# Performance work log

Hardware: AMD Instinct MI355X
Metric: run time of the kernel (lower is better)

## Reference

```python
import jax, jax.numpy as jnp
import numpy as np
import math

D_MODEL, D_K, N_HEADS = 1024, 64, 16
N, T = 2, 2048


def setup_inputs() -> dict:
    key = jax.random.key(0)
    ks = jax.random.split(key, 12)
    s = 1.0 / math.sqrt(D_MODEL)
    dh = D_K * N_HEADS
    return {
        "k": jax.random.normal(ks[0], (N, T, D_MODEL), jnp.float32),
        "q": jax.random.normal(ks[1], (N, T, D_MODEL), jnp.float32),
        "v": jax.random.normal(ks[2], (N, T, D_MODEL), jnp.float32),
        "mask": jnp.ones((N, T), jnp.int32),
        "Wk": jax.random.normal(ks[3], (D_MODEL, dh), jnp.float32) * s,
        "bk": jnp.zeros((dh,), jnp.float32),
        "Wq": jax.random.normal(ks[4], (D_MODEL, dh), jnp.float32) * s,
        "bq": jnp.zeros((dh,), jnp.float32),
        "Wv": jax.random.normal(ks[5], (D_MODEL, dh), jnp.float32) * s,
        "bv": jnp.zeros((dh,), jnp.float32),
        "Wo": jax.random.normal(ks[6], (dh, D_MODEL), jnp.float32) * (1.0 / math.sqrt(dh)),
        "bo": jnp.zeros((D_MODEL,), jnp.float32),
    }


def reference(k, q, v, mask, Wk, bk, Wq, bq, Wv, bv, Wo, bo):
    n, t = k.shape[0], k.shape[1]
    # project and split heads -> (N, H, T, d_k)
    K = (k @ Wk + bk).reshape(n, t, N_HEADS, D_K).transpose(0, 2, 1, 3)
    Q = (q @ Wq + bq).reshape(n, t, N_HEADS, D_K).transpose(0, 2, 1, 3)
    V = (v @ Wv + bv).reshape(n, t, N_HEADS, D_K).transpose(0, 2, 1, 3)
    scores = jnp.einsum("bhqd,bhkd->bhqk", Q, K) / math.sqrt(D_K)
    scores = jnp.where(mask[:, None, None, :] == 0, -jnp.inf, scores)
    weights = jax.nn.softmax(scores, axis=-1)
    A = jnp.einsum("bhqk,bhkd->bhqd", weights, V)
    A = A.transpose(0, 2, 1, 3).reshape(n, t, N_HEADS * D_K)
    return A @ Wo + bo
```

## Files before the change

### kernel.cpp

```cpp
#include <hip/hip_runtime.h>


typedef __bf16 bf16;
typedef __bf16 bf16x8 __attribute__((ext_vector_type(8)));
typedef __bf16 bf16x4 __attribute__((ext_vector_type(4)));
typedef float f32x4 __attribute__((ext_vector_type(4)));

#define MFMA16(a, b, c) __builtin_amdgcn_mfma_f32_16x16x32_bf16((a), (b), (c), 0, 0, 0)

__device__ __forceinline__ void load_lds16(const bf16* g, bf16* l) {
  __builtin_amdgcn_global_load_lds(
      (const __attribute__((address_space(1))) unsigned int*)g,
      (__attribute__((address_space(3))) unsigned int*)l, 16, 0, 0);
}

__device__ __forceinline__ bf16x8 cvt8(const float* __restrict__ p) {
  const f32x4 a = *(const f32x4*)p;
  const f32x4 b = *(const f32x4*)(p + 4);
  bf16x8 r;
  r[0] = (bf16)a[0]; r[1] = (bf16)a[1]; r[2] = (bf16)a[2]; r[3] = (bf16)a[3];
  r[4] = (bf16)b[0]; r[5] = (bf16)b[1]; r[6] = (bf16)b[2]; r[7] = (bf16)b[3];
  return r;
}

__global__ __launch_bounds__(256) void convert3(const float* __restrict__ a,
                                                const float* __restrict__ b,
                                                const float* __restrict__ c,
                                                bf16* __restrict__ oa,
                                                bf16* __restrict__ ob,
                                                bf16* __restrict__ oc) {
  const size_t i = ((size_t)blockIdx.x * 256 + threadIdx.x) * 8;
  const int which = (int)(i >> 22);
  const size_t off = i & ((size_t)(1u << 22) - 1);
  const float* src = which == 0 ? a : (which == 1 ? b : c);
  bf16* dst = which == 0 ? oa : (which == 1 ? ob : oc);
  *(bf16x8*)&dst[off] = cvt8(&src[off]);
}

__global__ __launch_bounds__(256) void transposeW(
    const float* __restrict__ W0, const float* __restrict__ W1,
    const float* __restrict__ W2, const float* __restrict__ W3,
    bf16* __restrict__ T0, bf16* __restrict__ T1, bf16* __restrict__ T2,
    bf16* __restrict__ T3) {
  __shared__ bf16 t[64 * 72];
  const int z = blockIdx.z;
  const float* W = z == 0 ? W0 : (z == 1 ? W1 : (z == 2 ? W2 : W3));
  bf16* T = z == 0 ? T0 : (z == 1 ? T1 : (z == 2 ? T2 : T3));
  const int kBase = blockIdx.y * 64, nBase = blockIdx.x * 64;
  const int tid = threadIdx.x;
  const int row = tid >> 2, cs = (tid & 3) * 16;

  const float* src = &W[(size_t)(kBase + row) * 1024 + nBase + cs];
  *(bf16x8*)&t[row * 72 + cs] = cvt8(src);
  *(bf16x8*)&t[row * 72 + cs + 8] = cvt8(src + 8);
  __syncthreads();

  const int n = tid >> 2, ks = (tid & 3) * 16;
  bf16 buf[16];
#pragma unroll
  for (int j = 0; j < 16; ++j) buf[j] = t[(ks + j) * 72 + n];
  bf16* dst = &T[(size_t)(nBase + n) * 1024 + kBase + ks];
  *(bf16x8*)&dst[0] = *(bf16x8*)&buf[0];
  *(bf16x8*)&dst[8] = *(bf16x8*)&buf[8];
}

__global__ __launch_bounds__(256) void gemm_qkv(
    const bf16* __restrict__ kb, const bf16* __restrict__ vb,
    const bf16* __restrict__ qb, const bf16* __restrict__ WkT,
    const bf16* __restrict__ WvT, const bf16* __restrict__ WqT,
    const float* __restrict__ bk, const float* __restrict__ bv,
    const float* __restrict__ bq, bf16* __restrict__ K_buf,
    bf16* __restrict__ Vt_buf, bf16* __restrict__ Q_buf) {
  __shared__ __align__(16) bf16 S[18432];
  bf16* As = S;
  bf16* Ws = S + 8192;
  const int tid = threadIdx.x;
  const int lane = tid & 63, w = tid >> 6;
  const int l15 = lane & 15, quad = lane >> 4;
  const int z = blockIdx.z;
  const bf16* X = z == 0 ? kb : (z == 1 ? vb : qb);
  const bf16* WT = z == 0 ? WkT : (z == 1 ? WvT : WqT);
  const float* B = z == 0 ? bk : (z == 1 ? bv : bq);
  const int mBase = blockIdx.y * 128, nBase = blockIdx.x * 128;
  const int wm = (w >> 1) * 64, wn = (w & 1) * 64;

  const int r8 = tid >> 3;
  const int jg = ((tid & 7) ^ (r8 & 7)) * 8;
  const int sw = l15 & 7;

  f32x4 acc[4][4] = {};

  for (int k0 = 0; k0 < 1024; k0 += 64) {
    __syncthreads();
#pragma unroll
    for (int i = 0; i < 4; ++i) {
      const int row = r8 + i * 32;
      load_lds16(&X[(size_t)(mBase + row) * 1024 + k0 + jg], &As[(tid + i * 256) * 8]);
      load_lds16(&WT[(size_t)(nBase + row) * 1024 + k0 + jg], &Ws[(tid + i * 256) * 8]);
    }
    __syncthreads();

#pragma unroll
    for (int k2 = 0; k2 < 2; ++k2) {
      const int col = ((k2 * 4 + quad) ^ sw) * 8;
      bf16x8 a[4], bb[4];
#pragma unroll
      for (int mt = 0; mt < 4; ++mt)
        a[mt] = *(const bf16x8*)&As[(wm + mt * 16 + l15) * 64 + col];
#pragma unroll
      for (int nt = 0; nt < 4; ++nt)
        bb[nt] = *(const bf16x8*)&Ws[(wn + nt * 16 + l15) * 64 + col];
#pragma unroll
      for (int mt = 0; mt < 4; ++mt)
#pragma unroll
        for (int nt = 0; nt < 4; ++nt)
          acc[mt][nt] = MFMA16(a[mt], bb[nt], acc[mt][nt]);
    }
  }

  if (z != 1) {
    const float scale = (z == 2) ? 0.125f : 1.0f;
    bf16* o = (z == 0) ? K_buf : Q_buf;
#pragma unroll
    for (int nt = 0; nt < 4; ++nt) {
      const int n = nBase + wn + nt * 16 + l15;
      const float bias = B[n];
      const int h = n >> 6, d = n & 63;
#pragma unroll
      for (int mt = 0; mt < 4; ++mt)
#pragma unroll
        for (int r = 0; r < 4; ++r) {
          const int m = mBase + wm + mt * 16 + quad * 4 + r;
          const int b = m >> 11, t = m & 2047;
          o[((size_t)(b * 16 + h) * 2048 + t) * 64 + d] =
              (bf16)((acc[mt][nt][r] + bias) * scale);
        }
    }
  } else {
    __syncthreads();
    bf16* Tb = &S[w * 4608];
#pragma unroll
    for (int nt = 0; nt < 4; ++nt) {
      const int n = nBase + wn + nt * 16 + l15;
      const float bias = B[n];
#pragma unroll
      for (int mt = 0; mt < 4; ++mt) {
        bf16x4 pk;
#pragma unroll
        for (int r = 0; r < 4; ++r) pk[r] = (bf16)(acc[mt][nt][r] + bias);
        *(bf16x4*)&Tb[(nt * 16 + l15) * 72 + mt * 16 + quad * 4] = pk;
      }
    }
    const int b = mBase >> 11;
#pragma unroll
    for (int i = 0; i < 8; ++i) {
      const int dl = i * 8 + (lane >> 3), ts = (lane & 7) * 8;
      const bf16x8 vv = *(const bf16x8*)&Tb[dl * 72 + ts];
      const int n = nBase + wn + dl;
      const int h = n >> 6, d = n & 63;
      const int t = (mBase + wm + ts) & 2047;
      *(bf16x8*)&Vt_buf[((size_t)(b * 16 + h) * 64 + d) * 2048 + t] = vv;
    }
  }
}

__global__ __launch_bounds__(256) void gemm_out(const bf16* __restrict__ X,
                                                const bf16* __restrict__ WT,
                                                const float* __restrict__ B,
                                                float* __restrict__ out) {
  __shared__ __align__(16) bf16 As[128 * 64];
  __shared__ __align__(16) bf16 Ws[64 * 64];
  const int tid = threadIdx.x;
  const int lane = tid & 63, w = tid >> 6;
  const int l15 = lane & 15, quad = lane >> 4;
  const int mBase = blockIdx.y * 128, nBase = blockIdx.x * 64;
  const int wm = (w >> 1) * 64, wn = (w & 1) * 32;

  const int r8 = tid >> 3;
  const int jg = ((tid & 7) ^ (r8 & 7)) * 8;
  const int sw = l15 & 7;

  f32x4 acc[4][2] = {};

  for (int k0 = 0; k0 < 1024; k0 += 64) {
    __syncthreads();
#pragma unroll
    for (int i = 0; i < 4; ++i)
      load_lds16(&X[(size_t)(mBase + r8 + i * 32) * 1024 + k0 + jg],
                 &As[(tid + i * 256) * 8]);
#pragma unroll
    for (int i = 0; i < 2; ++i)
      load_lds16(&WT[(size_t)(nBase + r8 + i * 32) * 1024 + k0 + jg],
                 &Ws[(tid + i * 256) * 8]);
    __syncthreads();

#pragma unroll
    for (int k2 = 0; k2 < 2; ++k2) {
      const int col = ((k2 * 4 + quad) ^ sw) * 8;
      bf16x8 a[4], bb[2];
#pragma unroll
      for (int mt = 0; mt < 4; ++mt)
        a[mt] = *(const bf16x8*)&As[(wm + mt * 16 + l15) * 64 + col];
#pragma unroll
      for (int nt = 0; nt < 2; ++nt)
        bb[nt] = *(const bf16x8*)&Ws[(wn + nt * 16 + l15) * 64 + col];
#pragma unroll
      for (int mt = 0; mt < 4; ++mt)
#pragma unroll
        for (int nt = 0; nt < 2; ++nt)
          acc[mt][nt] = MFMA16(a[mt], bb[nt], acc[mt][nt]);
    }
  }

#pragma unroll
  for (int nt = 0; nt < 2; ++nt) {
    const int n = nBase + wn + nt * 16 + l15;
    const float bias = B[n];
#pragma unroll
    for (int mt = 0; mt < 4; ++mt)
#pragma unroll
      for (int r = 0; r < 4; ++r) {
        const int m = mBase + wm + mt * 16 + quad * 4 + r;
        out[(size_t)m * 1024 + n] = acc[mt][nt][r] + bias;
      }
  }
}

__global__ __launch_bounds__(256) void flash_attn(const bf16* __restrict__ Q,
                                                  const bf16* __restrict__ K,
                                                  const bf16* __restrict__ Vt,
                                                  const int* __restrict__ mask,
                                                  bf16* __restrict__ A) {
  __shared__ __align__(16) bf16 Ks[64 * 64];
  __shared__ __align__(16) bf16 Vs[64 * 64];
  __shared__ __align__(16) bf16 Ps[64 * 72];
  __shared__ __align__(16) int msk[64];

  const int tid = threadIdx.x;
  const int lane = tid & 63, w = tid >> 6;
  const int l15 = lane & 15, quad = lane >> 4;
  const int bh = blockIdx.y;
  const int b = bh >> 4, h = bh & 15;
  const int qt = blockIdx.x * 64;

  const int r8 = tid >> 3;
  const int jg = ((tid & 7) ^ (r8 & 7)) * 8;
  const int sw = l15 & 7;

  const size_t qbase = ((size_t)bh * 2048 + qt + w * 16 + l15) * 64;
  const bf16x8 bq0 = *(const bf16x8*)&Q[qbase + quad * 8];
  const bf16x8 bq1 = *(const bf16x8*)&Q[qbase + 32 + quad * 8];

  f32x4 o[4] = {};
  float rs = 0.0f;

  for (int kt = 0; kt < 2048; kt += 64) {
    __syncthreads();
#pragma unroll
    for (int i = 0; i < 2; ++i) {
      const int row = r8 + i * 32;
      load_lds16(&K[((size_t)bh * 2048 + kt + row) * 64 + jg], &Ks[(tid + i * 256) * 8]);
      load_lds16(&Vt[((size_t)bh * 64 + row) * 2048 + kt + jg], &Vs[(tid + i * 256) * 8]);
    }
    if (tid < 64) msk[tid] = mask[b * 2048 + kt + tid];
    __syncthreads();

#pragma unroll
    for (int nt = 0; nt < 4; ++nt) {
      const bf16x8 ak0 = *(const bf16x8*)&Ks[(nt * 16 + l15) * 64 + ((quad ^ sw) * 8)];
      const bf16x8 ak1 = *(const bf16x8*)&Ks[(nt * 16 + l15) * 64 + (((4 + quad) ^ sw) * 8)];
      f32x4 s4 = {};
      s4 = MFMA16(ak0, bq0, s4);
      s4 = MFMA16(ak1, bq1, s4);
      const int4 mi = *(const int4*)&msk[nt * 16 + quad * 4];
      const float p0 = mi.x ? __expf(s4[0]) : 0.0f;
      const float p1 = mi.y ? __expf(s4[1]) : 0.0f;
      const float p2 = mi.z ? __expf(s4[2]) : 0.0f;
      const float p3 = mi.w ? __expf(s4[3]) : 0.0f;
      rs += (p0 + p1) + (p2 + p3);
      bf16x4 pk;
      pk[0] = (bf16)p0; pk[1] = (bf16)p1; pk[2] = (bf16)p2; pk[3] = (bf16)p3;
      *(bf16x4*)&Ps[(w * 16 + l15) * 72 + nt * 16 + quad * 4] = pk;
    }

#pragma unroll
    for (int ks = 0; ks < 2; ++ks) {
      const bf16x8 bp = *(const bf16x8*)&Ps[(w * 16 + l15) * 72 + ks * 32 + quad * 8];
#pragma unroll
      for (int mt = 0; mt < 4; ++mt) {
        const bf16x8 av =
            *(const bf16x8*)&Vs[(mt * 16 + l15) * 64 + (((ks * 4 + quad) ^ sw) * 8)];
        o[mt] = MFMA16(av, bp, o[mt]);
      }
    }
  }

  rs += __shfl_xor(rs, 16);
  rs += __shfl_xor(rs, 32);
  const float inv = rs > 0.0f ? 1.0f / rs : 0.0f;

  const int t = qt + w * 16 + l15;
  const size_t base = ((size_t)b * 2048 + t) * 1024 + h * 64;
#pragma unroll
  for (int mt = 0; mt < 4; ++mt) {
    bf16x4 ov;
#pragma unroll
    for (int r = 0; r < 4; ++r) ov[r] = (bf16)(o[mt][r] * inv);
    *(bf16x4*)&A[base + mt * 16 + quad * 4] = ov;
  }
}

extern "C" void kernel_launch(void* const* d_in, const int* in_sizes, int n_in,
                              void* d_out, int out_size, void* d_ws, size_t ws_size,
                              hipStream_t stream) {
  const float* k = (const float*)d_in[0];
  const float* q = (const float*)d_in[1];
  const float* v = (const float*)d_in[2];
  const int* mask = (const int*)d_in[3];
  const float* Wk = (const float*)d_in[4];
  const float* bk = (const float*)d_in[5];
  const float* Wq = (const float*)d_in[6];
  const float* bq = (const float*)d_in[7];
  const float* Wv = (const float*)d_in[8];
  const float* bv = (const float*)d_in[9];
  const float* Wo = (const float*)d_in[10];
  const float* bo = (const float*)d_in[11];

  const size_t ELEMS = (size_t)4 * 1024 * 1024;
  const size_t WELEMS = (size_t)1024 * 1024;

  bf16* kb = (bf16*)d_ws;
  bf16* qb = kb + ELEMS;
  bf16* vb = qb + ELEMS;
  bf16* WkT = vb + ELEMS;
  bf16* WqT = WkT + WELEMS;
  bf16* WvT = WqT + WELEMS;
  bf16* WoT = WvT + WELEMS;

  bf16* K_buf = (bf16*)d_in[0];
  bf16* Q_buf = (bf16*)d_in[0] + ELEMS;
  bf16* Vt_buf = (bf16*)d_in[2];
  bf16* A_buf = (bf16*)d_in[2] + ELEMS;

  convert3<<<6144, 256, 0, stream>>>(k, q, v, kb, qb, vb);
  transposeW<<<dim3(16, 16, 4), 256, 0, stream>>>(Wk, Wq, Wv, Wo,
                                                  WkT, WqT, WvT, WoT);
  gemm_qkv<<<dim3(8, 32, 3), 256, 0, stream>>>(kb, vb, qb, WkT, WvT, WqT,
                                               bk, bv, bq, K_buf, Vt_buf, Q_buf);
  flash_attn<<<dim3(32, 32), 256, 0, stream>>>(Q_buf, K_buf, Vt_buf, mask, A_buf);
  gemm_out<<<dim3(16, 32), 256, 0, stream>>>(A_buf, WoT, bo, (float*)d_out);
}
```

Baseline: 249.4 us.

## Double-buffer LDS tiles with async prefetch in GEMM and attention kernels

Each kernel's main loop now prefetches the next K-tile into a second LDS buffer via global_load_lds while computing on the current one. It waits with a partial vmcnt and raw barriers instead of two full __syncthreads per iteration. The attention kernel also preloads the whole mask row into LDS once. This overlaps global memory latency with MFMA work, at the cost of doubled LDS footprint, which may reduce occupancy.

```diff
diff --git a/kernel.cpp b/kernel.cpp
--- a/kernel.cpp
+++ b/kernel.cpp
@@ -71,9 +71,7 @@
     const float* __restrict__ bk, const float* __restrict__ bv,
     const float* __restrict__ bq, bf16* __restrict__ K_buf,
     bf16* __restrict__ Vt_buf, bf16* __restrict__ Q_buf) {
-  __shared__ __align__(16) bf16 S[18432];
-  bf16* As = S;
-  bf16* Ws = S + 8192;
+  __shared__ __align__(16) bf16 S[32768];
   const int tid = threadIdx.x;
   const int lane = tid & 63, w = tid >> 6;
   const int l15 = lane & 15, quad = lane >> 4;
@@ -90,33 +88,48 @@
 
   f32x4 acc[4][4] = {};
 
-  for (int k0 = 0; k0 < 1024; k0 += 64) {
-    __syncthreads();
+  auto issue8 = [&](int buf, int k0) {
 #pragma unroll
     for (int i = 0; i < 4; ++i) {
       const int row = r8 + i * 32;
-      load_lds16(&X[(size_t)(mBase + row) * 1024 + k0 + jg], &As[(tid + i * 256) * 8]);
-      load_lds16(&WT[(size_t)(nBase + row) * 1024 + k0 + jg], &Ws[(tid + i * 256) * 8]);
-    }
-    __syncthreads();
-
+      load_lds16(&X[(size_t)(mBase + row) * 1024 + k0 + jg],
+                 &S[buf * 8192 + (tid + i * 256) * 8]);
+      load_lds16(&WT[(size_t)(nBase + row) * 1024 + k0 + jg],
+                 &S[16384 + buf * 8192 + (tid + i * 256) * 8]);
+    }
+  };
+  auto compute = [&](int cur) {
+    const bf16* Ac = &S[cur * 8192];
+    const bf16* Wc = &S[16384 + cur * 8192];
 #pragma unroll
     for (int k2 = 0; k2 < 2; ++k2) {
       const int col = ((k2 * 4 + quad) ^ sw) * 8;
       bf16x8 a[4], bb[4];
 #pragma unroll
       for (int mt = 0; mt < 4; ++mt)
-        a[mt] = *(const bf16x8*)&As[(wm + mt * 16 + l15) * 64 + col];
+        a[mt] = *(const bf16x8*)&Ac[(wm + mt * 16 + l15) * 64 + col];
 #pragma unroll
       for (int nt = 0; nt < 4; ++nt)
-        bb[nt] = *(const bf16x8*)&Ws[(wn + nt * 16 + l15) * 64 + col];
+        bb[nt] = *(const bf16x8*)&Wc[(wn + nt * 16 + l15) * 64 + col];
 #pragma unroll
       for (int mt = 0; mt < 4; ++mt)
 #pragma unroll
         for (int nt = 0; nt < 4; ++nt)
           acc[mt][nt] = MFMA16(a[mt], bb[nt], acc[mt][nt]);
     }
-  }
+  };
+
+  issue8(0, 0);
+  for (int it = 0; it < 15; ++it) {
+    issue8((it + 1) & 1, (it + 1) * 64);
+    __builtin_amdgcn_s_waitcnt(0xF78);
+    __builtin_amdgcn_s_barrier();
+    compute(it & 1);
+    __builtin_amdgcn_s_barrier();
+  }
+  __builtin_amdgcn_s_waitcnt(0xF70);
+  __builtin_amdgcn_s_barrier();
+  compute(1);
 
   if (z != 1) {
     const float scale = (z == 2) ? 0.125f : 1.0f;
@@ -168,8 +181,7 @@
                                                 const bf16* __restrict__ WT,
                                                 const float* __restrict__ B,
                                                 float* __restrict__ out) {
-  __shared__ __align__(16) bf16 As[128 * 64];
-  __shared__ __align__(16) bf16 Ws[64 * 64];
+  __shared__ __align__(16) bf16 S[24576];
   const int tid = threadIdx.x;
   const int lane = tid & 63, w = tid >> 6;
   const int l15 = lane & 15, quad = lane >> 4;
@@ -182,35 +194,48 @@
 
   f32x4 acc[4][2] = {};
 
-  for (int k0 = 0; k0 < 1024; k0 += 64) {
-    __syncthreads();
+  auto issue6 = [&](int buf, int k0) {
 #pragma unroll
     for (int i = 0; i < 4; ++i)
       load_lds16(&X[(size_t)(mBase + r8 + i * 32) * 1024 + k0 + jg],
-                 &As[(tid + i * 256) * 8]);
+                 &S[buf * 8192 + (tid + i * 256) * 8]);
 #pragma unroll
     for (int i = 0; i < 2; ++i)
       load_lds16(&WT[(size_t)(nBase + r8 + i * 32) * 1024 + k0 + jg],
-                 &Ws[(tid + i * 256) * 8]);
-    __syncthreads();
-
+                 &S[16384 + buf * 4096 + (tid + i * 256) * 8]);
+  };
+  auto compute = [&](int cur) {
+    const bf16* Ac = &S[cur * 8192];
+    const bf16* Wc = &S[16384 + cur * 4096];
 #pragma unroll
     for (int k2 = 0; k2 < 2; ++k2) {
       const int col = ((k2 * 4 + quad) ^ sw) * 8;
       bf16x8 a[4], bb[2];
 #pragma unroll
       for (int mt = 0; mt < 4; ++mt)
-        a[mt] = *(const bf16x8*)&As[(wm + mt * 16 + l15) * 64 + col];
+        a[mt] = *(const bf16x8*)&Ac[(wm + mt * 16 + l15) * 64 + col];
 #pragma unroll
       for (int nt = 0; nt < 2; ++nt)
-        bb[nt] = *(const bf16x8*)&Ws[(wn + nt * 16 + l15) * 64 + col];
+        bb[nt] = *(const bf16x8*)&Wc[(wn + nt * 16 + l15) * 64 + col];
 #pragma unroll
       for (int mt = 0; mt < 4; ++mt)
 #pragma unroll
         for (int nt = 0; nt < 2; ++nt)
           acc[mt][nt] = MFMA16(a[mt], bb[nt], acc[mt][nt]);
     }
-  }
+  };
+
+  issue6(0, 0);
+  for (int it = 0; it < 15; ++it) {
+    issue6((it + 1) & 1, (it + 1) * 64);
+    __builtin_amdgcn_s_waitcnt(0xF76);
+    __builtin_amdgcn_s_barrier();
+    compute(it & 1);
+    __builtin_amdgcn_s_barrier();
+  }
+  __builtin_amdgcn_s_waitcnt(0xF70);
+  __builtin_amdgcn_s_barrier();
+  compute(1);
 
 #pragma unroll
   for (int nt = 0; nt < 2; ++nt) {
@@ -231,10 +256,10 @@
                                                   const bf16* __restrict__ Vt,
                                                   const int* __restrict__ mask,
                                                   bf16* __restrict__ A) {
-  __shared__ __align__(16) bf16 Ks[64 * 64];
-  __shared__ __align__(16) bf16 Vs[64 * 64];
+  __shared__ __align__(16) bf16 KsB[2 * 4096];
+  __shared__ __align__(16) bf16 VsB[2 * 4096];
   __shared__ __align__(16) bf16 Ps[64 * 72];
-  __shared__ __align__(16) int msk[64];
+  __shared__ __align__(16) int mskAll[2048];
 
   const int tid = threadIdx.x;
   const int lane = tid & 63, w = tid >> 6;
@@ -250,29 +275,37 @@
   const size_t qbase = ((size_t)bh * 2048 + qt + w * 16 + l15) * 64;
   const bf16x8 bq0 = *(const bf16x8*)&Q[qbase + quad * 8];
   const bf16x8 bq1 = *(const bf16x8*)&Q[qbase + 32 + quad * 8];
+  {
+    const int4* mrow = (const int4*)(mask + b * 2048);
+    *(int4*)&mskAll[tid * 8] = mrow[tid * 2];
+    *(int4*)&mskAll[tid * 8 + 4] = mrow[tid * 2 + 1];
+  }
+  __syncthreads();
 
   f32x4 o[4] = {};
   float rs = 0.0f;
 
-  for (int kt = 0; kt < 2048; kt += 64) {
-    __syncthreads();
+  auto issue4 = [&](int buf, int kt) {
 #pragma unroll
     for (int i = 0; i < 2; ++i) {
       const int row = r8 + i * 32;
-      load_lds16(&K[((size_t)bh * 2048 + kt + row) * 64 + jg], &Ks[(tid + i * 256) * 8]);
-      load_lds16(&Vt[((size_t)bh * 64 + row) * 2048 + kt + jg], &Vs[(tid + i * 256) * 8]);
-    }
-    if (tid < 64) msk[tid] = mask[b * 2048 + kt + tid];
-    __syncthreads();
-
+      load_lds16(&K[((size_t)bh * 2048 + kt + row) * 64 + jg],
+                 &KsB[buf * 4096 + (tid + i * 256) * 8]);
+      load_lds16(&Vt[((size_t)bh * 64 + row) * 2048 + kt + jg],
+                 &VsB[buf * 4096 + (tid + i * 256) * 8]);
+    }
+  };
+  auto tile = [&](int cur, int kt) {
+    const bf16* Kc = &KsB[cur * 4096];
+    const bf16* Vc = &VsB[cur * 4096];
 #pragma unroll
     for (int nt = 0; nt < 4; ++nt) {
-      const bf16x8 ak0 = *(const bf16x8*)&Ks[(nt * 16 + l15) * 64 + ((quad ^ sw) * 8)];
-      const bf16x8 ak1 = *(const bf16x8*)&Ks[(nt * 16 + l15) * 64 + (((4 + quad) ^ sw) * 8)];
+      const bf16x8 ak0 = *(const bf16x8*)&Kc[(nt * 16 + l15) * 64 + ((quad ^ sw) * 8)];
+      const bf16x8 ak1 = *(const bf16x8*)&Kc[(nt * 16 + l15) * 64 + (((4 + quad) ^ sw) * 8)];
       f32x4 s4 = {};
       s4 = MFMA16(ak0, bq0, s4);
       s4 = MFMA16(ak1, bq1, s4);
-      const int4 mi = *(const int4*)&msk[nt * 16 + quad * 4];
+      const int4 mi = *(const int4*)&mskAll[kt + nt * 16 + quad * 4];
       const float p0 = mi.x ? __expf(s4[0]) : 0.0f;
       const float p1 = mi.y ? __expf(s4[1]) : 0.0f;
       const float p2 = mi.z ? __expf(s4[2]) : 0.0f;
@@ -282,18 +315,29 @@
       pk[0] = (bf16)p0; pk[1] = (bf16)p1; pk[2] = (bf16)p2; pk[3] = (bf16)p3;
       *(bf16x4*)&Ps[(w * 16 + l15) * 72 + nt * 16 + quad * 4] = pk;
     }
-
 #pragma unroll
     for (int ks = 0; ks < 2; ++ks) {
       const bf16x8 bp = *(const bf16x8*)&Ps[(w * 16 + l15) * 72 + ks * 32 + quad * 8];
 #pragma unroll
       for (int mt = 0; mt < 4; ++mt) {
         const bf16x8 av =
-            *(const bf16x8*)&Vs[(mt * 16 + l15) * 64 + (((ks * 4 + quad) ^ sw) * 8)];
+            *(const bf16x8*)&Vc[(mt * 16 + l15) * 64 + (((ks * 4 + quad) ^ sw) * 8)];
         o[mt] = MFMA16(av, bp, o[mt]);
       }
     }
-  }
+  };
+
+  issue4(0, 0);
+  for (int it = 0; it < 31; ++it) {
+    issue4((it + 1) & 1, (it + 1) * 64);
+    __builtin_amdgcn_s_waitcnt(0xF74);
+    __builtin_amdgcn_s_barrier();
+    tile(it & 1, it * 64);
+    __builtin_amdgcn_s_barrier();
+  }
+  __builtin_amdgcn_s_waitcnt(0xF70);
+  __builtin_amdgcn_s_barrier();
+  tile(1, 31 * 64);
 
   rs += __shfl_xor(rs, 16);
   rs += __shfl_xor(rs, 32);
```

Measured after the change: 250.9 us. No clear change (+0.6%).
